# Optimization experiments

Hardware: AMD Instinct MI355X
Metric: run time of the kernel (lower is better)

## Reference

```python
import jax, jax.numpy as jnp
import numpy as np

N_NODES = 50000
N_EDGES = 800000
D_IN = 128
D_OUT = 128
N_TYPES = 4
LN_EPS = 1e-5


def setup_inputs() -> dict:
    key = jax.random.key(0)
    ks = jax.random.split(key, 12)
    s1 = 1.0 / np.sqrt(2 * D_IN)
    s2 = 1.0 / np.sqrt(D_OUT)
    return {
        "x": jax.random.normal(ks[0], (N_NODES, D_IN), jnp.float32),
        "edge_index": jax.random.randint(ks[1], (2, N_EDGES), 0, N_NODES, jnp.int32),
        "edge_attr": jax.random.randint(ks[2], (N_EDGES,), 0, N_TYPES, jnp.int32),
        # per-edge-type 2-layer MLP params, stacked over type axis
        "edge_w1": jax.random.uniform(ks[3], (N_TYPES, 2 * D_IN, D_OUT), jnp.float32, -s1, s1),
        "edge_b1": jax.random.uniform(ks[4], (N_TYPES, D_OUT), jnp.float32, -s1, s1),
        "edge_w2": jax.random.uniform(ks[5], (N_TYPES, D_OUT, D_OUT), jnp.float32, -s2, s2),
        "edge_b2": jax.random.uniform(ks[6], (N_TYPES, D_OUT), jnp.float32, -s2, s2),
        "self_w": jax.random.uniform(ks[7], (D_IN, D_OUT), jnp.float32, -s2, s2),
        "self_b": jax.random.uniform(ks[8], (D_OUT,), jnp.float32, -s2, s2),
        "ln_gamma": jnp.ones((D_OUT,), jnp.float32),
        "ln_beta": jnp.zeros((D_OUT,), jnp.float32),
    }


def reference(x, edge_index, edge_attr, edge_w1, edge_b1, edge_w2, edge_b2, self_w, self_b, ln_gamma, ln_beta):
    row, col = edge_index[0], edge_index[1]
    out = x @ self_w + self_b  # (N, D_OUT) self-loop

    # gather once: (E, 2*D_IN)
    ef = jnp.concatenate([x[row], x[col]], axis=1)

    # per-edge-type MLP; masked edges contribute exactly zero, matching the
    # boolean-mask + index_add_ semantics of the original.
    msg = jnp.zeros((ef.shape[0], edge_w2.shape[-1]), dtype=x.dtype)
    for t in range(edge_w1.shape[0]):
        h = jax.nn.relu(ef @ edge_w1[t] + edge_b1[t])
        m = h @ edge_w2[t] + edge_b2[t]
        msg = msg + jnp.where((edge_attr == t)[:, None], m, 0.0)

    out = out + jax.ops.segment_sum(msg, col, num_segments=x.shape[0])

    # ReLU then LayerNorm over feature dim
    h = jax.nn.relu(out)
    mu = jnp.mean(h, axis=-1, keepdims=True)
    var = jnp.mean(jnp.square(h - mu), axis=-1, keepdims=True)
    return (h - mu) * jax.lax.rsqrt(var + LN_EPS) * ln_gamma + ln_beta
```

## Files before the change

kernel.cpp:

```cpp
#include <hip/hip_runtime.h>

#define N_NODES 50000
#define N_EDGES 800000
#define D_IN 128
#define D_OUT 128
#define N_TYPES 4
#define LN_EPS 1e-5f
#define N_BUCKETS (N_TYPES * N_NODES)
#define NJT 9

#define NBIN 196
#define BIN_CAP 8192
#define TILE_A 2048
#define NBA ((N_EDGES + TILE_A - 1) / TILE_A)

typedef __attribute__((ext_vector_type(4))) float f32x4;
typedef __attribute__((ext_vector_type(8))) __bf16 bf16x8;
typedef __attribute__((ext_vector_type(8))) unsigned short u16x8;

constexpr size_t wsal(size_t x) { return (x + 255) & ~size_t(255); }
constexpr size_t OFF_PTR    = 0;
constexpr size_t OFF_BCUR   = OFF_PTR   + wsal((size_t)(N_BUCKETS + 1) * 4);
constexpr size_t OFF_BINBUF = OFF_BCUR  + wsal((size_t)256 * 4);
constexpr size_t OFF_SROWS  = OFF_BINBUF + wsal((size_t)NBIN * BIN_CAP * 4);
constexpr size_t OFF_XB     = OFF_SROWS + wsal((size_t)N_EDGES * 4);
constexpr size_t OFF_WCAT   = OFF_XB    + wsal((size_t)N_NODES * D_IN * 2);
constexpr size_t OFF_BIAS   = OFF_WCAT  + wsal((size_t)NJT * 4 * 128 * 32 * 2);
constexpr size_t OFF_W2T    = OFF_BIAS  + wsal((size_t)NJT * 128 * 4);
constexpr size_t OFF_XAB    = OFF_W2T   + wsal((size_t)N_TYPES * 4 * 128 * 32 * 2);
constexpr size_t OFF_S      = OFF_XAB   + wsal((size_t)8 * N_NODES * 128 * 2);
constexpr size_t WS_TOTAL   = OFF_S     + wsal((size_t)N_BUCKETS * 128 * 2);

__device__ __forceinline__ unsigned short f2bf(float f) {
    unsigned int u = __builtin_bit_cast(unsigned int, f);
    u += 0x7FFFu + ((u >> 16) & 1u);
    return (unsigned short)(u >> 16);
}
__device__ __forceinline__ float bf2f_lo(unsigned int u) { return __builtin_bit_cast(float, u << 16); }
__device__ __forceinline__ float bf2f_hi(unsigned int u) { return __builtin_bit_cast(float, u & 0xFFFF0000u); }

#define PREP_N0 (NJT * 4 * 128 * 32)
#define PREP_N1 (NJT * 128)
#define PREP_N2 (N_TYPES * 4 * 128 * 32)
#define NB_CVT  (N_NODES * D_IN / 4 / 256)
#define NB_PREP ((PREP_N0 + PREP_N1 + PREP_N2 + 255) / 256)

__global__ __launch_bounds__(256) void k_prep_all(
    const float* __restrict__ x,
    const float* __restrict__ w1, const float* __restrict__ sw,
    const float* __restrict__ b1, const float* __restrict__ sb,
    const float* __restrict__ w2,
    unsigned short* __restrict__ xb,
    unsigned short* __restrict__ wcatT, float* __restrict__ bias,
    unsigned short* __restrict__ w2T)
{
    const int bx = blockIdx.x;
    const int tid = threadIdx.x;
    if (bx < NB_CVT) {
        int i = bx * 256 + tid;
        const float4 v = reinterpret_cast<const float4*>(x)[i];
        ushort4 o;
        o.x = f2bf(v.x); o.y = f2bf(v.y); o.z = f2bf(v.z); o.w = f2bf(v.w);
        reinterpret_cast<ushort4*>(xb)[i] = o;
        return;
    }
    int gid = (bx - NB_CVT) * 256 + tid;
    if (gid < PREP_N0) {
        int kk = gid & 31;
        int jm = (gid >> 5) & 127;
        int ks = (gid >> 12) & 3;
        int jt = gid >> 14;
        int k  = ks * 32 + kk;
        float v;
        if (jt < 8) {
            int t = jt >> 1, half = jt & 1;
            v = w1[((size_t)t * 256 + half * 128 + k) * 128 + jm];
        } else {
            v = sw[(size_t)k * 128 + jm];
        }
        wcatT[gid] = f2bf(v);
        return;
    }
    gid -= PREP_N0;
    if (gid < PREP_N1) {
        int jt = gid >> 7, jm = gid & 127;
        float v = 0.f;
        if (jt < 8) { if (jt & 1) v = b1[(jt >> 1) * 128 + jm]; }
        else v = sb[jm];
        bias[gid] = v;
        return;
    }
    gid -= PREP_N1;
    if (gid < PREP_N2) {
        int kk = gid & 31;
        int f  = (gid >> 5) & 127;
        int ks = (gid >> 12) & 3;
        int t  = gid >> 14;
        float v = w2[((size_t)t * 128 + ks * 32 + kk) * 128 + f];
        w2T[gid] = f2bf(v);
    }
}

__global__ __launch_bounds__(256) void k_binA(
    const int* __restrict__ ei, const int* __restrict__ attr,
    int* __restrict__ binCur, unsigned int* __restrict__ binBuf)
{
    __shared__ int hist[NBIN];
    __shared__ int base[NBIN];
    const int tid = threadIdx.x;
    const int e0 = blockIdx.x * TILE_A;
    if (tid < NBIN) hist[tid] = 0;
    __syncthreads();
    #pragma unroll
    for (int it = 0; it < TILE_A / 256; ++it) {
        int e = e0 + it * 256 + tid;
        if (e < N_EDGES) atomicAdd(&hist[ei[N_EDGES + e] >> 8], 1);
    }
    __syncthreads();
    if (tid < NBIN) {
        base[tid] = atomicAdd(&binCur[tid], hist[tid]);
        hist[tid] = 0;
    }
    __syncthreads();
    #pragma unroll
    for (int it = 0; it < TILE_A / 256; ++it) {
        int e = e0 + it * 256 + tid;
        if (e < N_EDGES) {
            int c = ei[N_EDGES + e];
            int t = attr[e];
            int row = ei[e];
            int bin = c >> 8;
            int lr = atomicAdd(&hist[bin], 1);
            int dst = base[bin] + lr;
            unsigned int rec = ((unsigned int)(c & 255) << 21) | ((unsigned int)t << 19)
                             | (unsigned int)(2 * t * N_NODES + row);
            if (dst < BIN_CAP) binBuf[(size_t)bin * BIN_CAP + dst] = rec;
        }
    }
}

__global__ __launch_bounds__(256) void k_binB(
    const unsigned int* __restrict__ binBuf, const int* __restrict__ binCur,
    int* __restrict__ ptr, int* __restrict__ srows)
{
    __shared__ unsigned int recs[BIN_CAP];
    __shared__ int stage[BIN_CAP];
    __shared__ int boff[1024];
    __shared__ int sred[256];
    const int b = blockIdx.x, tid = threadIdx.x;
    const int cntb = min(binCur[b], BIN_CAP);

    for (int i = tid; i < cntb; i += 256)
        recs[i] = binBuf[(size_t)b * BIN_CAP + i];

    int myv = (tid < NBIN && tid < b) ? binCur[tid] : 0;
    sred[tid] = myv;
    __syncthreads();
    #pragma unroll
    for (int d = 128; d > 0; d >>= 1) {
        if (tid < d) sred[tid] += sred[tid + d];
        __syncthreads();
    }
    const int binBase = sred[0];
    __syncthreads();

    for (int k = tid; k < 1024; k += 256) boff[k] = 0;
    __syncthreads();
    for (int i = tid; i < cntb; i += 256)
        atomicAdd(&boff[(recs[i] >> 19) & 1023], 1);
    __syncthreads();

    const int c0 = boff[tid * 4], c1 = boff[tid * 4 + 1], c2 = boff[tid * 4 + 2], c3 = boff[tid * 4 + 3];
    const int ts = c0 + c1 + c2 + c3;
    sred[tid] = ts;
    __syncthreads();
    #pragma unroll
    for (int d = 1; d < 256; d <<= 1) {
        int add = (tid >= d) ? sred[tid - d] : 0;
        __syncthreads();
        sred[tid] += add;
        __syncthreads();
    }
    const int run = sred[tid] - ts;
    const int o0 = run, o1 = run + c0, o2 = run + c0 + c1, o3 = run + c0 + c1 + c2;
    boff[tid * 4 + 0] = o0; boff[tid * 4 + 1] = o1;
    boff[tid * 4 + 2] = o2; boff[tid * 4 + 3] = o3;
    const int gb = b * 1024 + tid * 4;
    if (gb + 3 < N_BUCKETS) {
        int4 pv; pv.x = binBase + o0; pv.y = binBase + o1; pv.z = binBase + o2; pv.w = binBase + o3;
        *reinterpret_cast<int4*>(ptr + gb) = pv;
    } else {
        if (gb + 0 < N_BUCKETS) ptr[gb + 0] = binBase + o0;
        if (gb + 1 < N_BUCKETS) ptr[gb + 1] = binBase + o1;
        if (gb + 2 < N_BUCKETS) ptr[gb + 2] = binBase + o2;
        if (gb + 3 < N_BUCKETS) ptr[gb + 3] = binBase + o3;
    }
    if (b == 0 && tid == 0) ptr[N_BUCKETS] = N_EDGES;
    __syncthreads();

    for (int i = tid; i < cntb; i += 256) {
        unsigned int r = recs[i];
        int pos = atomicAdd(&boff[(r >> 19) & 1023], 1);
        stage[pos] = (int)(r & 0x7FFFFu);
    }
    __syncthreads();
    for (int i = tid; i < cntb; i += 256)
        srows[binBase + i] = stage[i];
}

__global__ __launch_bounds__(256, 2) void k_gemm1(
    const unsigned short* __restrict__ xb,
    const unsigned short* __restrict__ wcatT,
    const float* __restrict__ bias,
    unsigned short* __restrict__ xab)
{
    const int nb = blockIdx.x * 128;

    __shared__ __align__(16) unsigned short sX[128 * 136];
    __shared__ __align__(16) unsigned short sW[128 * 136];

    const int tid = threadIdx.x;
    const int lane = tid & 63;
    const int w = tid >> 6;
    const int g = lane >> 4;
    const int c = lane & 15;
    const int wf = w >> 1;
    const int we = w & 1;

    #pragma unroll
    for (int it = 0; it < 8; ++it) {
        int row = 16 * it + (tid >> 4);
        int node = min(nb + row, N_NODES - 1);
        const u16x8 v = *reinterpret_cast<const u16x8*>(xb + (size_t)node * D_IN + (tid & 15) * 8);
        *reinterpret_cast<u16x8*>(&sX[row * 136 + (tid & 15) * 8]) = v;
    }

    u16x8 wreg[8];
    {
        const u16x8* gsrc = reinterpret_cast<const u16x8*>(wcatT);
        #pragma unroll
        for (int i = 0; i < 8; ++i) wreg[i] = gsrc[i * 256 + tid];
    }

    for (int jt = 0; jt < 8; ++jt) {
        #pragma unroll
        for (int i = 0; i < 8; ++i) {
            int idx = i * 256 + tid;
            int ks = idx >> 9, f = (idx >> 2) & 127, k8 = idx & 3;
            *reinterpret_cast<u16x8*>(&sW[f * 136 + ks * 32 + k8 * 8]) = wreg[i];
        }
        if (jt < 7) {
            const u16x8* gsrc = reinterpret_cast<const u16x8*>(wcatT + (size_t)(jt + 1) * 16384);
            #pragma unroll
            for (int i = 0; i < 8; ++i) wreg[i] = gsrc[i * 256 + tid];
        }
        __syncthreads();

        f32x4 acc[4][4];
        #pragma unroll
        for (int ft = 0; ft < 4; ++ft)
            #pragma unroll
            for (int et = 0; et < 4; ++et)
                acc[ft][et] = f32x4{0.f, 0.f, 0.f, 0.f};

        #pragma unroll
        for (int ks = 0; ks < 4; ++ks) {
            bf16x8 af[4], bfr[4];
            #pragma unroll
            for (int ft = 0; ft < 4; ++ft)
                af[ft] = *reinterpret_cast<const bf16x8*>(&sW[(64 * wf + 16 * ft + c) * 136 + ks * 32 + 8 * g]);
            #pragma unroll
            for (int et = 0; et < 4; ++et)
                bfr[et] = *reinterpret_cast<const bf16x8*>(&sX[(64 * we + 16 * et + c) * 136 + ks * 32 + 8 * g]);
            #pragma unroll
            for (int ft = 0; ft < 4; ++ft)
                #pragma unroll
                for (int et = 0; et < 4; ++et)
                    acc[ft][et] = __builtin_amdgcn_mfma_f32_16x16x32_bf16(af[ft], bfr[et], acc[ft][et], 0, 0, 0);
        }

        float bv[4][4];
        #pragma unroll
        for (int ft = 0; ft < 4; ++ft)
            #pragma unroll
            for (int r = 0; r < 4; ++r)
                bv[ft][r] = bias[jt * 128 + 64 * wf + 16 * ft + 4 * g + r];
        #pragma unroll
        for (int et = 0; et < 4; ++et) {
            int n = 64 * we + 16 * et + c;
            int node = nb + n;
            if (node < N_NODES) {
                unsigned int* orow = reinterpret_cast<unsigned int*>(
                    xab + ((size_t)jt * N_NODES + node) * 128);
                #pragma unroll
                for (int ft = 0; ft < 4; ++ft) {
                    int f0 = 64 * wf + 16 * ft + 4 * g;
                    uint2 pk;
                    pk.x = (unsigned int)f2bf(acc[ft][et][0] + bv[ft][0])
                         | ((unsigned int)f2bf(acc[ft][et][1] + bv[ft][1]) << 16);
                    pk.y = (unsigned int)f2bf(acc[ft][et][2] + bv[ft][2])
                         | ((unsigned int)f2bf(acc[ft][et][3] + bv[ft][3]) << 16);
                    *reinterpret_cast<uint2*>(orow + (f0 >> 1)) = pk;
                }
            }
        }
        __syncthreads();
    }
}

__global__ __launch_bounds__(256) void k_agg(const unsigned short* __restrict__ xab,
                                             const int* __restrict__ ptr,
                                             const int* __restrict__ srows,
                                             unsigned short* __restrict__ S)
{
    const int n = (blockIdx.x * 256 + threadIdx.x) >> 6;
    if (n >= N_NODES) return;
    const int lane = threadIdx.x & 63;
    const unsigned int* x32 = reinterpret_cast<const unsigned int*>(xab);

    int seg[5];
    #pragma unroll
    for (int t = 0; t < 5; ++t)
        seg[t] = __builtin_amdgcn_readfirstlane(ptr[4 * n + t]);

    float xbl[4], xbh[4];
    #pragma unroll
    for (int t = 0; t < 4; ++t) {
        unsigned int v = x32[((size_t)(2 * t + 1) * N_NODES + n) * 64 + lane];
        xbl[t] = bf2f_lo(v); xbh[t] = bf2f_hi(v);
    }

    float al[4] = {0.f, 0.f, 0.f, 0.f}, ah[4] = {0.f, 0.f, 0.f, 0.f};

    const int p0 = seg[0], pE = seg[4];
    for (int co = p0; co < pE; co += 64) {
        const int rem = pE - co;
        const int cv = srows[co + min(lane, rem - 1)];
        const int ce = min(co + 64, pE);
        #pragma unroll
        for (int t = 0; t < 4; ++t) {
            const int lo = max(seg[t], co);
            const int hi = min(seg[t + 1], ce);
            int j = lo;
            for (; j + 4 <= hi; j += 4) {
                int a0 = __builtin_amdgcn_readlane(cv, j - co);
                int a1 = __builtin_amdgcn_readlane(cv, j + 1 - co);
                int a2 = __builtin_amdgcn_readlane(cv, j + 2 - co);
                int a3 = __builtin_amdgcn_readlane(cv, j + 3 - co);
                unsigned int v0 = x32[(size_t)a0 * 64 + lane];
                unsigned int v1 = x32[(size_t)a1 * 64 + lane];
                unsigned int v2 = x32[(size_t)a2 * 64 + lane];
                unsigned int v3 = x32[(size_t)a3 * 64 + lane];
                al[t] += fmaxf(bf2f_lo(v0) + xbl[t], 0.f) + fmaxf(bf2f_lo(v1) + xbl[t], 0.f)
                       + fmaxf(bf2f_lo(v2) + xbl[t], 0.f) + fmaxf(bf2f_lo(v3) + xbl[t], 0.f);
                ah[t] += fmaxf(bf2f_hi(v0) + xbh[t], 0.f) + fmaxf(bf2f_hi(v1) + xbh[t], 0.f)
                       + fmaxf(bf2f_hi(v2) + xbh[t], 0.f) + fmaxf(bf2f_hi(v3) + xbh[t], 0.f);
            }
            for (; j < hi; ++j) {
                int a = __builtin_amdgcn_readlane(cv, j - co);
                unsigned int v = x32[(size_t)a * 64 + lane];
                al[t] += fmaxf(bf2f_lo(v) + xbl[t], 0.f);
                ah[t] += fmaxf(bf2f_hi(v) + xbh[t], 0.f);
            }
        }
    }

    unsigned int* S32 = reinterpret_cast<unsigned int*>(S);
    #pragma unroll
    for (int t = 0; t < 4; ++t)
        S32[((size_t)n * 4 + t) * 64 + lane] =
            (unsigned int)f2bf(al[t]) | ((unsigned int)f2bf(ah[t]) << 16);
}

__global__ __launch_bounds__(256, 2) void k_gemm2_ln(
    const unsigned short* __restrict__ S,
    const unsigned short* __restrict__ w2T,
    const unsigned short* __restrict__ wcatT,
    const unsigned short* __restrict__ xb,
    const float* __restrict__ b2,
    const float* __restrict__ sb,
    const int* __restrict__ ptr,
    const float* __restrict__ gamma,
    const float* __restrict__ beta,
    float* __restrict__ out)
{
    const int nb = blockIdx.x * 128;
    __shared__ __align__(16) unsigned char sm[128 * 136 * 2 + 4 * 128 * 32 * 2 + 512 * 4];
    unsigned short* sS  = reinterpret_cast<unsigned short*>(sm);
    unsigned short* sW2 = reinterpret_cast<unsigned short*>(sm + 34816);
    float* sB2          = reinterpret_cast<float*>(sm + 34816 + 32768);
    float* rows         = reinterpret_cast<float*>(sm);

    const int tid = threadIdx.x;
    const int lane = tid & 63;
    const int w = tid >> 6;
    const int g = lane >> 4;
    const int c = lane & 15;
    const int wf = w >> 1;
    const int we = w & 1;

    sB2[tid] = b2[tid];
    sB2[tid + 256] = b2[tid + 256];

    f32x4 acc[4][4];
    #pragma unroll
    for (int ft = 0; ft < 4; ++ft)
        #pragma unroll
        for (int et = 0; et < 4; ++et)
            acc[ft][et] = f32x4{0.f, 0.f, 0.f, 0.f};

    u16x8 sreg[8], wreg[8];
    {
        #pragma unroll
        for (int it = 0; it < 8; ++it) {
            int row = 16 * it + (tid >> 4);
            int node = min(nb + row, N_NODES - 1);
            sreg[it] = *reinterpret_cast<const u16x8*>(S + ((size_t)node * 4 + 0) * 128 + (tid & 15) * 8);
        }
        const u16x8* gsrc = reinterpret_cast<const u16x8*>(w2T);
        #pragma unroll
        for (int it = 0; it < 8; ++it)
            wreg[it] = gsrc[it * 256 + tid];
    }

    for (int t = 0; t < 5; ++t) {
        #pragma unroll
        for (int it = 0; it < 8; ++it) {
            int row = 16 * it + (tid >> 4);
            *reinterpret_cast<u16x8*>(&sS[row * 136 + (tid & 15) * 8]) = sreg[it];
        }
        {
            u16x8* ldst = reinterpret_cast<u16x8*>(sW2);
            #pragma unroll
            for (int it = 0; it < 8; ++it)
                ldst[tid + 256 * it] = wreg[it];
        }
        if (t < 4) {
            #pragma unroll
            for (int it = 0; it < 8; ++it) {
                int row = 16 * it + (tid >> 4);
                int node = min(nb + row, N_NODES - 1);
                const unsigned short* src = (t + 1 < 4)
                    ? S + ((size_t)node * 4 + (t + 1)) * 128
                    : xb + (size_t)node * 128;
                sreg[it] = *reinterpret_cast<const u16x8*>(src + (tid & 15) * 8);
            }
            const unsigned short* srcW = (t + 1 < 4) ? w2T + (size_t)(t + 1) * 16384
                                                     : wcatT + (size_t)8 * 16384;
            const u16x8* gsrc = reinterpret_cast<const u16x8*>(srcW);
            #pragma unroll
            for (int it = 0; it < 8; ++it)
                wreg[it] = gsrc[it * 256 + tid];
        }
        __syncthreads();
        #pragma unroll
        for (int ks = 0; ks < 4; ++ks) {
            bf16x8 af[4], bfr[4];
            #pragma unroll
            for (int ft = 0; ft < 4; ++ft)
                af[ft] = *reinterpret_cast<const bf16x8*>(&sW2[ks * 4096 + (64 * wf + 16 * ft + c) * 32 + 8 * g]);
            #pragma unroll
            for (int et = 0; et < 4; ++et)
                bfr[et] = *reinterpret_cast<const bf16x8*>(&sS[(64 * we + 16 * et + c) * 136 + ks * 32 + 8 * g]);
            #pragma unroll
            for (int ft = 0; ft < 4; ++ft)
                #pragma unroll
                for (int et = 0; et < 4; ++et)
                    acc[ft][et] = __builtin_amdgcn_mfma_f32_16x16x32_bf16(af[ft], bfr[et], acc[ft][et], 0, 0, 0);
        }
        __syncthreads();
    }

    #pragma unroll
    for (int et = 0; et < 4; ++et) {
        int n = 64 * we + 16 * et + c;
        int node = nb + n;
        if (node >= N_NODES) continue;
        const int4 pv4 = *reinterpret_cast<const int4*>(ptr + node * 4);
        const int pe = ptr[node * 4 + 4];
        float cnt4[N_TYPES] = {(float)(pv4.y - pv4.x), (float)(pv4.z - pv4.y),
                               (float)(pv4.w - pv4.z), (float)(pe - pv4.w)};
        #pragma unroll
        for (int ft = 0; ft < 4; ++ft) {
            int f0 = 64 * wf + 16 * ft + 4 * g;
            const float4 sbv = *reinterpret_cast<const float4*>(sb + f0);
            float v[4];
            v[0] = acc[ft][et][0] + sbv.x;
            v[1] = acc[ft][et][1] + sbv.y;
            v[2] = acc[ft][et][2] + sbv.z;
            v[3] = acc[ft][et][3] + sbv.w;
            #pragma unroll
            for (int r = 0; r < 4; ++r) {
                float bs = 0.f;
                #pragma unroll
                for (int t = 0; t < N_TYPES; ++t)
                    bs = fmaf(cnt4[t], sB2[t * 128 + f0 + r], bs);
                v[r] += bs;
            }
            *reinterpret_cast<float4*>(&rows[n * 132 + f0]) = *reinterpret_cast<float4*>(v);
        }
    }
    __syncthreads();

    for (int rr = 0; rr < 32; ++rr) {
        int r = w * 32 + rr;
        int node = nb + r;
        if (node >= N_NODES) break;
        float2 v = *reinterpret_cast<float2*>(&rows[r * 132 + lane * 2]);
        v.x = fmaxf(v.x, 0.f);
        v.y = fmaxf(v.y, 0.f);
        float s = v.x + v.y;
        float ss = v.x * v.x + v.y * v.y;
        #pragma unroll
        for (int m = 1; m < 64; m <<= 1) {
            s  += __shfl_xor(s, m, 64);
            ss += __shfl_xor(ss, m, 64);
        }
        float mu = s * (1.f / 128.f);
        float var = ss * (1.f / 128.f) - mu * mu;
        float rs = rsqrtf(var + LN_EPS);
        const float2 gm = *reinterpret_cast<const float2*>(gamma + lane * 2);
        const float2 bt = *reinterpret_cast<const float2*>(beta + lane * 2);
        float2 o;
        o.x = (v.x - mu) * rs * gm.x + bt.x;
        o.y = (v.y - mu) * rs * gm.y + bt.y;
        *reinterpret_cast<float2*>(out + (size_t)node * D_OUT + lane * 2) = o;
    }
}

extern "C" void kernel_launch(void* const* d_in, const int* in_sizes, int n_in,
                              void* d_out, int out_size, void* d_ws, size_t ws_size,
                              hipStream_t stream) {
    const float* x     = (const float*)d_in[0];
    const int*   ei    = (const int*)d_in[1];
    const int*   attr  = (const int*)d_in[2];
    const float* w1    = (const float*)d_in[3];
    const float* b1    = (const float*)d_in[4];
    const float* w2    = (const float*)d_in[5];
    const float* b2    = (const float*)d_in[6];
    const float* sw    = (const float*)d_in[7];
    const float* sb    = (const float*)d_in[8];
    const float* gamma = (const float*)d_in[9];
    const float* beta  = (const float*)d_in[10];
    float* out = (float*)d_out;

    if (ws_size < WS_TOTAL) return;

    char* ws = (char*)d_ws;
    int* ptr    = (int*)(ws + OFF_PTR);
    int* binCur = (int*)(ws + OFF_BCUR);
    unsigned int* binBuf = (unsigned int*)(ws + OFF_BINBUF);
    int* srows  = (int*)(ws + OFF_SROWS);
    unsigned short* xb    = (unsigned short*)(ws + OFF_XB);
    unsigned short* wcatT = (unsigned short*)(ws + OFF_WCAT);
    float*          bias  = (float*)(ws + OFF_BIAS);
    unsigned short* w2T   = (unsigned short*)(ws + OFF_W2T);
    unsigned short* xab   = (unsigned short*)(ws + OFF_XAB);
    unsigned short* S     = (unsigned short*)(ws + OFF_S);

    hipMemsetAsync(binCur, 0, (size_t)NBIN * 4, stream);

    k_prep_all<<<NB_CVT + NB_PREP, 256, 0, stream>>>(
        x, w1, sw, b1, sb, w2, xb, wcatT, bias, w2T);

    k_binA<<<NBA, 256, 0, stream>>>(ei, attr, binCur, binBuf);
    k_binB<<<NBIN, 256, 0, stream>>>(binBuf, binCur, ptr, srows);

    k_gemm1<<<(N_NODES + 127) / 128, 256, 0, stream>>>(xb, wcatT, bias, xab);
    k_agg<<<(N_NODES * 64 + 255) / 256, 256, 0, stream>>>(xab, ptr, srows, S);
    k_gemm2_ln<<<(N_NODES + 127) / 128, 256, 0, stream>>>(
        S, w2T, wcatT, xb, b2, sb, ptr, gamma, beta, out);
}
```

Measured before the change: 168.8 us.

## Merge prep with binA and binB with a 2D-gridded gemm1

Combines the independent preprocessing and edge-binning phase-A work into one launch, and runs bin phase B alongside gemm1 in a shared launch. gemm1 now gives each block a single 128-column weight tile, so the grid is 8x wider and the serial jt loop goes away. Its output is staged through LDS so global stores are coalesced. In gemm2 a barrier moves ahead of the next-tile prefetch. The aim is fewer kernel launches and serial tails and more parallelism, at the cost of re-reading each x tile 8 times and using 69KB of LDS per block.

```diff
diff --git a/kernel.cpp b/kernel.cpp
--- a/kernel.cpp
+++ b/kernel.cpp
@@ -13,6 +13,8 @@
 #define BIN_CAP 8192
 #define TILE_A 2048
 #define NBA ((N_EDGES + TILE_A - 1) / TILE_A)
+
+#define G1_NX ((N_NODES + 127) / 128)
 
 typedef __attribute__((ext_vector_type(4))) float f32x4;
 typedef __attribute__((ext_vector_type(8))) __bf16 bf16x8;
@@ -45,26 +47,65 @@
 #define NB_CVT  (N_NODES * D_IN / 4 / 256)
 #define NB_PREP ((PREP_N0 + PREP_N1 + PREP_N2 + 255) / 256)
 
-__global__ __launch_bounds__(256) void k_prep_all(
+__global__ __launch_bounds__(256) void k_prep_binA(
     const float* __restrict__ x,
     const float* __restrict__ w1, const float* __restrict__ sw,
     const float* __restrict__ b1, const float* __restrict__ sb,
     const float* __restrict__ w2,
+    const int* __restrict__ ei, const int* __restrict__ attr,
     unsigned short* __restrict__ xb,
     unsigned short* __restrict__ wcatT, float* __restrict__ bias,
-    unsigned short* __restrict__ w2T)
+    unsigned short* __restrict__ w2T,
+    int* __restrict__ binCur, unsigned int* __restrict__ binBuf)
 {
+    __shared__ int sm[2 * NBIN];
     const int bx = blockIdx.x;
     const int tid = threadIdx.x;
-    if (bx < NB_CVT) {
-        int i = bx * 256 + tid;
+
+    if (bx < NBA) {
+        int* hist = sm;
+        int* base = sm + NBIN;
+        const int e0 = bx * TILE_A;
+        if (tid < NBIN) hist[tid] = 0;
+        __syncthreads();
+        #pragma unroll
+        for (int it = 0; it < TILE_A / 256; ++it) {
+            int e = e0 + it * 256 + tid;
+            if (e < N_EDGES) atomicAdd(&hist[ei[N_EDGES + e] >> 8], 1);
+        }
+        __syncthreads();
+        if (tid < NBIN) {
+            base[tid] = atomicAdd(&binCur[tid], hist[tid]);
+            hist[tid] = 0;
+        }
+        __syncthreads();
+        #pragma unroll
+        for (int it = 0; it < TILE_A / 256; ++it) {
+            int e = e0 + it * 256 + tid;
+            if (e < N_EDGES) {
+                int c = ei[N_EDGES + e];
+                int t = attr[e];
+                int row = ei[e];
+                int bin = c >> 8;
+                int lr = atomicAdd(&hist[bin], 1);
+                int dst = base[bin] + lr;
+                unsigned int rec = ((unsigned int)(c & 255) << 21) | ((unsigned int)t << 19)
+                                 | (unsigned int)(2 * t * N_NODES + row);
+                if (dst < BIN_CAP) binBuf[(size_t)bin * BIN_CAP + dst] = rec;
+            }
+        }
+        return;
+    }
+    const int pb = bx - NBA;
+    if (pb < NB_CVT) {
+        int i = pb * 256 + tid;
         const float4 v = reinterpret_cast<const float4*>(x)[i];
         ushort4 o;
         o.x = f2bf(v.x); o.y = f2bf(v.y); o.z = f2bf(v.z); o.w = f2bf(v.w);
         reinterpret_cast<ushort4*>(xb)[i] = o;
         return;
     }
-    int gid = (bx - NB_CVT) * 256 + tid;
+    int gid = (pb - NB_CVT) * 256 + tid;
     if (gid < PREP_N0) {
         int kk = gid & 31;
         int jm = (gid >> 5) & 127;
@@ -101,160 +142,114 @@
     }
 }
 
-__global__ __launch_bounds__(256) void k_binA(
-    const int* __restrict__ ei, const int* __restrict__ attr,
-    int* __restrict__ binCur, unsigned int* __restrict__ binBuf)
-{
-    __shared__ int hist[NBIN];
-    __shared__ int base[NBIN];
-    const int tid = threadIdx.x;
-    const int e0 = blockIdx.x * TILE_A;
-    if (tid < NBIN) hist[tid] = 0;
-    __syncthreads();
-    #pragma unroll
-    for (int it = 0; it < TILE_A / 256; ++it) {
-        int e = e0 + it * 256 + tid;
-        if (e < N_EDGES) atomicAdd(&hist[ei[N_EDGES + e] >> 8], 1);
-    }
-    __syncthreads();
-    if (tid < NBIN) {
-        base[tid] = atomicAdd(&binCur[tid], hist[tid]);
-        hist[tid] = 0;
-    }
-    __syncthreads();
-    #pragma unroll
-    for (int it = 0; it < TILE_A / 256; ++it) {
-        int e = e0 + it * 256 + tid;
-        if (e < N_EDGES) {
-            int c = ei[N_EDGES + e];
-            int t = attr[e];
-            int row = ei[e];
-            int bin = c >> 8;
-            int lr = atomicAdd(&hist[bin], 1);
-            int dst = base[bin] + lr;
-            unsigned int rec = ((unsigned int)(c & 255) << 21) | ((unsigned int)t << 19)
-                             | (unsigned int)(2 * t * N_NODES + row);
-            if (dst < BIN_CAP) binBuf[(size_t)bin * BIN_CAP + dst] = rec;
-        }
-    }
-}
-
-__global__ __launch_bounds__(256) void k_binB(
+__global__ __launch_bounds__(256, 2) void k_binB_gemm1(
     const unsigned int* __restrict__ binBuf, const int* __restrict__ binCur,
-    int* __restrict__ ptr, int* __restrict__ srows)
-{
-    __shared__ unsigned int recs[BIN_CAP];
-    __shared__ int stage[BIN_CAP];
-    __shared__ int boff[1024];
-    __shared__ int sred[256];
-    const int b = blockIdx.x, tid = threadIdx.x;
-    const int cntb = min(binCur[b], BIN_CAP);
-
-    for (int i = tid; i < cntb; i += 256)
-        recs[i] = binBuf[(size_t)b * BIN_CAP + i];
-
-    int myv = (tid < NBIN && tid < b) ? binCur[tid] : 0;
-    sred[tid] = myv;
-    __syncthreads();
-    #pragma unroll
-    for (int d = 128; d > 0; d >>= 1) {
-        if (tid < d) sred[tid] += sred[tid + d];
-        __syncthreads();
-    }
-    const int binBase = sred[0];
-    __syncthreads();
-
-    for (int k = tid; k < 1024; k += 256) boff[k] = 0;
-    __syncthreads();
-    for (int i = tid; i < cntb; i += 256)
-        atomicAdd(&boff[(recs[i] >> 19) & 1023], 1);
-    __syncthreads();
-
-    const int c0 = boff[tid * 4], c1 = boff[tid * 4 + 1], c2 = boff[tid * 4 + 2], c3 = boff[tid * 4 + 3];
-    const int ts = c0 + c1 + c2 + c3;
-    sred[tid] = ts;
-    __syncthreads();
-    #pragma unroll
-    for (int d = 1; d < 256; d <<= 1) {
-        int add = (tid >= d) ? sred[tid - d] : 0;
-        __syncthreads();
-        sred[tid] += add;
-        __syncthreads();
-    }
-    const int run = sred[tid] - ts;
-    const int o0 = run, o1 = run + c0, o2 = run + c0 + c1, o3 = run + c0 + c1 + c2;
-    boff[tid * 4 + 0] = o0; boff[tid * 4 + 1] = o1;
-    boff[tid * 4 + 2] = o2; boff[tid * 4 + 3] = o3;
-    const int gb = b * 1024 + tid * 4;
-    if (gb + 3 < N_BUCKETS) {
-        int4 pv; pv.x = binBase + o0; pv.y = binBase + o1; pv.z = binBase + o2; pv.w = binBase + o3;
-        *reinterpret_cast<int4*>(ptr + gb) = pv;
-    } else {
-        if (gb + 0 < N_BUCKETS) ptr[gb + 0] = binBase + o0;
-        if (gb + 1 < N_BUCKETS) ptr[gb + 1] = binBase + o1;
-        if (gb + 2 < N_BUCKETS) ptr[gb + 2] = binBase + o2;
-        if (gb + 3 < N_BUCKETS) ptr[gb + 3] = binBase + o3;
-    }
-    if (b == 0 && tid == 0) ptr[N_BUCKETS] = N_EDGES;
-    __syncthreads();
-
-    for (int i = tid; i < cntb; i += 256) {
-        unsigned int r = recs[i];
-        int pos = atomicAdd(&boff[(r >> 19) & 1023], 1);
-        stage[pos] = (int)(r & 0x7FFFFu);
-    }
-    __syncthreads();
-    for (int i = tid; i < cntb; i += 256)
-        srows[binBase + i] = stage[i];
-}
-
-__global__ __launch_bounds__(256, 2) void k_gemm1(
+    int* __restrict__ ptr, int* __restrict__ srows,
     const unsigned short* __restrict__ xb,
     const unsigned short* __restrict__ wcatT,
     const float* __restrict__ bias,
     unsigned short* __restrict__ xab)
 {
-    const int nb = blockIdx.x * 128;
-
-    __shared__ __align__(16) unsigned short sX[128 * 136];
-    __shared__ __align__(16) unsigned short sW[128 * 136];
-
+    __shared__ __align__(16) unsigned char smem[70656];
+    const int bx = blockIdx.x;
     const int tid = threadIdx.x;
-    const int lane = tid & 63;
-    const int w = tid >> 6;
-    const int g = lane >> 4;
-    const int c = lane & 15;
-    const int wf = w >> 1;
-    const int we = w & 1;
-
-    #pragma unroll
-    for (int it = 0; it < 8; ++it) {
-        int row = 16 * it + (tid >> 4);
-        int node = min(nb + row, N_NODES - 1);
-        const u16x8 v = *reinterpret_cast<const u16x8*>(xb + (size_t)node * D_IN + (tid & 15) * 8);
-        *reinterpret_cast<u16x8*>(&sX[row * 136 + (tid & 15) * 8]) = v;
-    }
-
-    u16x8 wreg[8];
+
+    if (bx < NBIN) {
+        unsigned int* recs = reinterpret_cast<unsigned int*>(smem);
+        int* stage = reinterpret_cast<int*>(smem + 32768);
+        int* boff  = reinterpret_cast<int*>(smem + 65536);
+        int* sred  = reinterpret_cast<int*>(smem + 69632);
+        const int b = bx;
+        const int cntb = min(binCur[b], BIN_CAP);
+
+        for (int i = tid; i < cntb; i += 256)
+            recs[i] = binBuf[(size_t)b * BIN_CAP + i];
+
+        int myv = (tid < NBIN && tid < b) ? binCur[tid] : 0;
+        sred[tid] = myv;
+        __syncthreads();
+        #pragma unroll
+        for (int d = 128; d > 0; d >>= 1) {
+            if (tid < d) sred[tid] += sred[tid + d];
+            __syncthreads();
+        }
+        const int binBase = sred[0];
+        __syncthreads();
+
+        for (int k = tid; k < 1024; k += 256) boff[k] = 0;
+        __syncthreads();
+        for (int i = tid; i < cntb; i += 256)
+            atomicAdd(&boff[(recs[i] >> 19) & 1023], 1);
+        __syncthreads();
+
+        const int c0 = boff[tid * 4], c1 = boff[tid * 4 + 1], c2 = boff[tid * 4 + 2], c3 = boff[tid * 4 + 3];
+        const int ts = c0 + c1 + c2 + c3;
+        sred[tid] = ts;
+        __syncthreads();
+        #pragma unroll
+        for (int d = 1; d < 256; d <<= 1) {
+            int add = (tid >= d) ? sred[tid - d] : 0;
+            __syncthreads();
+            sred[tid] += add;
+            __syncthreads();
+        }
+        const int run = sred[tid] - ts;
+        const int o0 = run, o1 = run + c0, o2 = run + c0 + c1, o3 = run + c0 + c1 + c2;
+        boff[tid * 4 + 0] = o0; boff[tid * 4 + 1] = o1;
+        boff[tid * 4 + 2] = o2; boff[tid * 4 + 3] = o3;
+        const int gb = b * 1024 + tid * 4;
+        if (gb + 3 < N_BUCKETS) {
+            int4 pv; pv.x = binBase + o0; pv.y = binBase + o1; pv.z = binBase + o2; pv.w = binBase + o3;
+            *reinterpret_cast<int4*>(ptr + gb) = pv;
+        } else {
+            if (gb + 0 < N_BUCKETS) ptr[gb + 0] = binBase + o0;
+            if (gb + 1 < N_BUCKETS) ptr[gb + 1] = binBase + o1;
+            if (gb + 2 < N_BUCKETS) ptr[gb + 2] = binBase + o2;
+            if (gb + 3 < N_BUCKETS) ptr[gb + 3] = binBase + o3;
+        }
+        if (b == 0 && tid == 0) ptr[N_BUCKETS] = N_EDGES;
+        __syncthreads();
+
+        for (int i = tid; i < cntb; i += 256) {
+            unsigned int r = recs[i];
+            int pos = atomicAdd(&boff[(r >> 19) & 1023], 1);
+            stage[pos] = (int)(r & 0x7FFFFu);
+        }
+        __syncthreads();
+        for (int i = tid; i < cntb; i += 256)
+            srows[binBase + i] = stage[i];
+        return;
+    }
+
     {
-        const u16x8* gsrc = reinterpret_cast<const u16x8*>(wcatT);
-        #pragma unroll
-        for (int i = 0; i < 8; ++i) wreg[i] = gsrc[i * 256 + tid];
-    }
-
-    for (int jt = 0; jt < 8; ++jt) {
-        #pragma unroll
-        for (int i = 0; i < 8; ++i) {
-            int idx = i * 256 + tid;
-            int ks = idx >> 9, f = (idx >> 2) & 127, k8 = idx & 3;
-            *reinterpret_cast<u16x8*>(&sW[f * 136 + ks * 32 + k8 * 8]) = wreg[i];
-        }
-        if (jt < 7) {
-            const u16x8* gsrc = reinterpret_cast<const u16x8*>(wcatT + (size_t)(jt + 1) * 16384);
-            #pragma unroll
-            for (int i = 0; i < 8; ++i) wreg[i] = gsrc[i * 256 + tid];
-        }
-        __syncthreads();
+        const int gbk = bx - NBIN;
+        const int nb = (gbk % G1_NX) * 128;
+        const int jt = gbk / G1_NX;
+
+        unsigned short* sX = reinterpret_cast<unsigned short*>(smem);
+        unsigned short* sW = reinterpret_cast<unsigned short*>(smem + 34816);
+
+        const int lane = tid & 63;
+        const int w = tid >> 6;
+        const int g = lane >> 4;
+        const int c = lane & 15;
+        const int wf = w >> 1;
+        const int we = w & 1;
+
+        #pragma unroll
+        for (int it = 0; it < 8; ++it) {
+            int row = 16 * it + (tid >> 4);
+            int node = min(nb + row, N_NODES - 1);
+            const u16x8 v = *reinterpret_cast<const u16x8*>(xb + (size_t)node * D_IN + (tid & 15) * 8);
+            *reinterpret_cast<u16x8*>(&sX[row * 136 + (tid & 15) * 8]) = v;
+        }
+        {
+            const u16x8* gsrc = reinterpret_cast<const u16x8*>(wcatT + (size_t)jt * 16384);
+            u16x8* ldst = reinterpret_cast<u16x8*>(sW);
+            #pragma unroll
+            for (int it = 0; it < 8; ++it)
+                ldst[tid + 256 * it] = gsrc[tid + 256 * it];
+        }
 
         f32x4 acc[4][4];
         #pragma unroll
@@ -263,12 +258,14 @@
             for (int et = 0; et < 4; ++et)
                 acc[ft][et] = f32x4{0.f, 0.f, 0.f, 0.f};
 
+        __syncthreads();
+
         #pragma unroll
         for (int ks = 0; ks < 4; ++ks) {
             bf16x8 af[4], bfr[4];
             #pragma unroll
             for (int ft = 0; ft < 4; ++ft)
-                af[ft] = *reinterpret_cast<const bf16x8*>(&sW[(64 * wf + 16 * ft + c) * 136 + ks * 32 + 8 * g]);
+                af[ft] = *reinterpret_cast<const bf16x8*>(&sW[ks * 4096 + (64 * wf + 16 * ft + c) * 32 + 8 * g]);
             #pragma unroll
             for (int et = 0; et < 4; ++et)
                 bfr[et] = *reinterpret_cast<const bf16x8*>(&sX[(64 * we + 16 * et + c) * 136 + ks * 32 + 8 * g]);
@@ -278,33 +275,42 @@
                 for (int et = 0; et < 4; ++et)
                     acc[ft][et] = __builtin_amdgcn_mfma_f32_16x16x32_bf16(af[ft], bfr[et], acc[ft][et], 0, 0, 0);
         }
-
-        float bv[4][4];
-        #pragma unroll
-        for (int ft = 0; ft < 4; ++ft)
-            #pragma unroll
-            for (int r = 0; r < 4; ++r)
-                bv[ft][r] = bias[jt * 128 + 64 * wf + 16 * ft + 4 * g + r];
-        #pragma unroll
-        for (int et = 0; et < 4; ++et) {
-            int n = 64 * we + 16 * et + c;
-            int node = nb + n;
+        __syncthreads();
+
+        {
+            float bv[4][4];
+            #pragma unroll
+            for (int ft = 0; ft < 4; ++ft)
+                #pragma unroll
+                for (int r = 0; r < 4; ++r)
+                    bv[ft][r] = bias[jt * 128 + 64 * wf + 16 * ft + 4 * g + r];
+            unsigned int* so = reinterpret_cast<unsigned int*>(sX);
+            #pragma unroll
+            for (int ft = 0; ft < 4; ++ft) {
+                #pragma unroll
+                for (int et = 0; et < 4; ++et) {
+                    int n = 64 * we + 16 * et + c;
+                    int jb = 32 * wf + 8 * ft + 2 * g;
+                    float v0 = acc[ft][et][0] + bv[ft][0];
+                    float v1 = acc[ft][et][1] + bv[ft][1];
+                    float v2 = acc[ft][et][2] + bv[ft][2];
+                    float v3 = acc[ft][et][3] + bv[ft][3];
+                    so[n * 68 + jb + 0] = (unsigned int)f2bf(v0) | ((unsigned int)f2bf(v1) << 16);
+                    so[n * 68 + jb + 1] = (unsigned int)f2bf(v2) | ((unsigned int)f2bf(v3) << 16);
+                }
+            }
+        }
+        __syncthreads();
+
+        #pragma unroll
+        for (int it = 0; it < 8; ++it) {
+            int row = 16 * it + (tid >> 4);
+            int node = nb + row;
             if (node < N_NODES) {
-                unsigned int* orow = reinterpret_cast<unsigned int*>(
-                    xab + ((size_t)jt * N_NODES + node) * 128);
-                #pragma unroll
-                for (int ft = 0; ft < 4; ++ft) {
-                    int f0 = 64 * wf + 16 * ft + 4 * g;
-                    uint2 pk;
-                    pk.x = (unsigned int)f2bf(acc[ft][et][0] + bv[ft][0])
-                         | ((unsigned int)f2bf(acc[ft][et][1] + bv[ft][1]) << 16);
-                    pk.y = (unsigned int)f2bf(acc[ft][et][2] + bv[ft][2])
-                         | ((unsigned int)f2bf(acc[ft][et][3] + bv[ft][3]) << 16);
-                    *reinterpret_cast<uint2*>(orow + (f0 >> 1)) = pk;
-                }
-            }
-        }
-        __syncthreads();
+                const u16x8 v = *reinterpret_cast<const u16x8*>(&sX[row * 136 + (tid & 15) * 8]);
+                *reinterpret_cast<u16x8*>(xab + ((size_t)jt * N_NODES + node) * 128 + (tid & 15) * 8) = v;
+            }
+        }
     }
 }
 
@@ -435,6 +441,8 @@
             for (int it = 0; it < 8; ++it)
                 ldst[tid + 256 * it] = wreg[it];
         }
+        __syncthreads();
+
         if (t < 4) {
             #pragma unroll
             for (int it = 0; it < 8; ++it) {
@@ -452,7 +460,6 @@
             for (int it = 0; it < 8; ++it)
                 wreg[it] = gsrc[it * 256 + tid];
         }
-        __syncthreads();
         #pragma unroll
         for (int ks = 0; ks < 4; ++ks) {
             bf16x8 af[4], bfr[4];
@@ -560,13 +567,12 @@
 
     hipMemsetAsync(binCur, 0, (size_t)NBIN * 4, stream);
 
-    k_prep_all<<<NB_CVT + NB_PREP, 256, 0, stream>>>(
-        x, w1, sw, b1, sb, w2, xb, wcatT, bias, w2T);
-
-    k_binA<<<NBA, 256, 0, stream>>>(ei, attr, binCur, binBuf);
-    k_binB<<<NBIN, 256, 0, stream>>>(binBuf, binCur, ptr, srows);
-
-    k_gemm1<<<(N_NODES + 127) / 128, 256, 0, stream>>>(xb, wcatT, bias, xab);
+    k_prep_binA<<<NBA + NB_CVT + NB_PREP, 256, 0, stream>>>(
+        x, w1, sw, b1, sb, w2, ei, attr, xb, wcatT, bias, w2T, binCur, binBuf);
+
+    k_binB_gemm1<<<NBIN + G1_NX * 8, 256, 0, stream>>>(
+        binBuf, binCur, ptr, srows, xb, wcatT, bias, xab);
+
     k_agg<<<(N_NODES * 64 + 255) / 256, 256, 0, stream>>>(xab, ptr, srows, S);
     k_gemm2_ln<<<(N_NODES + 127) / 128, 256, 0, stream>>>(
         S, w2T, wcatT, xb, b2, sb, ptr, gamma, beta, out);
```

Result: faster. 145.3 us, median of 2 (-13.9%).
